# Kernel optimization log

Hardware: AMD Instinct MI355X
Metric: run time of the kernel (lower is better)

## Reference

```python
import math
import jax, jax.numpy as jnp
import numpy as np

B, QDIM, KDIM, EMBED, HEADS, H, W = 2, 192, 192, 256, 8, 48, 48


def setup_inputs() -> dict:
    key = jax.random.key(0)
    ks = jax.random.split(key, 8)
    s = 0.05
    return {
        "query": jax.random.normal(ks[0], (B, QDIM, H, W), dtype=jnp.float32),
        "key": jax.random.normal(ks[1], (B, KDIM, H, W), dtype=jnp.float32),
        "Wq": jax.random.normal(ks[2], (EMBED, QDIM), dtype=jnp.float32) * s,
        "bq": jax.random.normal(ks[3], (EMBED,), dtype=jnp.float32) * s,
        "Wk": jax.random.normal(ks[4], (EMBED, KDIM), dtype=jnp.float32) * s,
        "bk": jax.random.normal(ks[5], (EMBED,), dtype=jnp.float32) * s,
        "Wv": jax.random.normal(ks[6], (EMBED, KDIM), dtype=jnp.float32) * s,
        "bv": jax.random.normal(ks[7], (EMBED,), dtype=jnp.float32) * s,
        "num_heads": HEADS,
    }


def reference(query, key, Wq, bq, Wk, bk, Wv, bv, num_heads):
    b, qdim, h, w = query.shape
    L = h * w
    embed = Wq.shape[0]
    hd = embed // num_heads

    # (B, C, H, W) -> (B, L, C) raster order
    q = query.transpose(0, 2, 3, 1).reshape(b, L, qdim)
    k_in = key.transpose(0, 2, 3, 1).reshape(b, L, -1)

    q = q @ Wq.T + bq               # (B, L, E)
    v = k_in @ Wv.T + bv            # (B, L, E)
    k = k_in @ Wk.T + bk            # (B, L, E)

    q = q.reshape(b, L, num_heads, hd).transpose(0, 2, 1, 3)  # bhqd
    k = k.reshape(b, L, num_heads, hd).transpose(0, 2, 1, 3)  # bhkd
    v = v.reshape(b, L, num_heads, hd).transpose(0, 2, 1, 3)  # bhkd

    scores = jnp.einsum("bhqd,bhkd->bhqk", q, k) / math.sqrt(hd)
    # causal (square subsequent) mask: -inf strictly above diagonal
    idx = jnp.arange(L)
    neg = jnp.asarray(jnp.finfo(scores.dtype).min, scores.dtype)
    mask = jnp.where(idx[:, None] >= idx[None, :], jnp.zeros((), scores.dtype), neg)
    scores = scores + mask

    attn = jax.nn.softmax(scores, axis=-1)  # dropout p=0.0 (eval)
    x = jnp.einsum("bhqk,bhkd->bhqd", attn, v)  # (B, H, L, hd)

    # (B, H, L, hd) -> (B, H, hd, L) -> (B, E, h, w)
    out = x.transpose(0, 1, 3, 2).reshape(b, embed, h, w)
    return out
```

## Files before the change

### kernel.cpp

```cpp
#include <hip/hip_runtime.h>

#define LQ 2304
#define CIN 192
#define EMB 256
#define NH 8
#define HD 32

typedef __attribute__((ext_vector_type(8))) short short8;
typedef __attribute__((ext_vector_type(4))) short short4v;
typedef __attribute__((ext_vector_type(4))) float floatx4;
typedef __attribute__((ext_vector_type(16))) float f32x16;

__device__ __forceinline__ unsigned short f2bf(float f) {
  union { float f; unsigned u; } v; v.f = f;
  unsigned r = v.u + 0x7FFFu + ((v.u >> 16) & 1u);
  return (unsigned short)(r >> 16);
}
__device__ __forceinline__ unsigned cvtpk(float lo, float hi) {
  unsigned r;
  asm("v_cvt_pk_bf16_f32 %0, %1, %2" : "=v"(r) : "v"(lo), "v"(hi));
  return r;
}
__device__ __forceinline__ void plswap(unsigned& a, unsigned& b, int hi) {
#if __has_builtin(__builtin_amdgcn_permlane32_swap)
  auto r = __builtin_amdgcn_permlane32_swap((int)a, (int)b, false, false);
  a = (unsigned)r[0]; b = (unsigned)r[1];
#else
  unsigned pa = (unsigned)__shfl_xor((int)a, 32);
  unsigned pb = (unsigned)__shfl_xor((int)b, 32);
  unsigned na = hi ? pb : a;
  unsigned nb = hi ? b : pa;
  a = na; b = nb;
#endif
}
__device__ __forceinline__ float xmax(float x, int hi) {
  unsigned a = __float_as_uint(x), b = a;
  plswap(a, b, hi);
  return fmaxf(__uint_as_float(a), __uint_as_float(b));
}
__device__ __forceinline__ float xadd(float x, int hi) {
  unsigned a = __float_as_uint(x), b = a;
  plswap(a, b, hi);
  return __uint_as_float(a) + __uint_as_float(b);
}

__global__ void k_prep(const float* __restrict__ q, const float* __restrict__ k,
                       const float* __restrict__ Wq, const float* __restrict__ Wk,
                       const float* __restrict__ Wv,
                       unsigned short* Xtq, unsigned short* Xtk,
                       unsigned short* Wqb, unsigned short* Wkb, unsigned short* Wvb) {
  if (blockIdx.z == 2) {
    const int n = EMB * CIN;
    int i = (blockIdx.x + 108 * blockIdx.y) * 256 + threadIdx.x;
    if (i < n) { Wqb[i] = f2bf(Wq[i]); Wkb[i] = f2bf(Wk[i]); Wvb[i] = f2bf(Wv[i]); }
    return;
  }
  __shared__ float tile[64][65];
  const float* src = blockIdx.z ? k : q;
  unsigned short* dst = blockIdx.z ? Xtk : Xtq;
  int b = blockIdx.y;
  int lt = blockIdx.x % 36, ct = blockIdx.x / 36;
  int l0 = lt * 64, c0 = ct * 64;
  int j = threadIdx.x & 63, i0 = threadIdx.x >> 6;
  const float* s = src + (size_t)b * CIN * LQ;
  for (int i = i0; i < 64; i += 4)
    tile[i][j] = s[(size_t)(c0 + i) * LQ + l0 + j];
  __syncthreads();
  unsigned short* d = dst + (size_t)b * LQ * CIN;
  for (int li = i0; li < 64; li += 4)
    d[(size_t)(l0 + li) * CIN + c0 + j] = f2bf(tile[j][li]);
}

__global__ __launch_bounds__(256) void k_proj(
    const unsigned short* __restrict__ Xtq, const unsigned short* __restrict__ Xtk,
    const unsigned short* __restrict__ Wqb, const unsigned short* __restrict__ Wkb,
    const unsigned short* __restrict__ Wvb,
    const float* __restrict__ bq, const float* __restrict__ bk, const float* __restrict__ bv,
    unsigned short* Qb, unsigned short* Kb, unsigned short* Vt) {
  int proj = blockIdx.z;
  int b = blockIdx.y;
  int l0 = blockIdx.x * 16;
  const unsigned short* Xt = (proj == 0) ? Xtq : Xtk;
  const unsigned short* W  = (proj == 0) ? Wqb : (proj == 1 ? Wkb : Wvb);
  const float* bias        = (proj == 0) ? bq  : (proj == 1 ? bk  : bv);
  const float alpha = (proj == 0) ? 0.25505653582177047f : 1.0f;

  int lane = threadIdx.x & 63, w = threadIdx.x >> 6;
  int g = lane >> 4, r16 = lane & 15;
  int e0 = w * 64;
  int lg = l0 + r16;

  floatx4 acc[4];
  #pragma unroll
  for (int a = 0; a < 4; ++a) acc[a] = (floatx4){0.f, 0.f, 0.f, 0.f};

  const unsigned short* xrow = Xt + ((size_t)b * LQ + lg) * CIN + g * 8;
  #pragma unroll
  for (int ks = 0; ks < CIN; ks += 32) {
    short8 xf = *(const short8*)(xrow + ks);
    #pragma unroll
    for (int a = 0; a < 4; ++a) {
      short8 wf = *(const short8*)(W + (size_t)(e0 + a * 16 + r16) * CIN + ks + g * 8);
      acc[a] = __builtin_amdgcn_mfma_f32_16x16x32_bf16(wf, xf, acc[a], 0, 0, 0);
    }
  }

  #pragma unroll
  for (int a = 0; a < 4; ++a) {
    int ebase = e0 + a * 16 + g * 4;
    int h = ebase >> 5, d0 = ebase & 31;
    if (proj < 2) {
      unsigned short* outp = (proj == 0) ? Qb : Kb;
      short4v pk;
      #pragma unroll
      for (int r = 0; r < 4; ++r)
        pk[r] = (short)f2bf((acc[a][r] + bias[ebase + r]) * alpha);
      *(short4v*)(outp + ((size_t)(b * NH + h) * LQ + lg) * HD + d0) = pk;
    } else {
      #pragma unroll
      for (int r = 0; r < 4; ++r)
        Vt[((size_t)(b * NH + h) * HD + d0 + r) * LQ + lg] =
            f2bf(acc[a][r] + bias[ebase + r]);
    }
  }
}

__global__ __launch_bounds__(256, 3) void k_attn(const unsigned short* __restrict__ Qb,
                                                 const unsigned short* __restrict__ Kb,
                                                 const unsigned short* __restrict__ Vt,
                                                 float* __restrict__ out) {
  __shared__ float Osh[4][32][33];
  __shared__ float Msh[4][32];
  __shared__ float Ssh[4][32];

  int bid = blockIdx.x;
  int xcd = bid & 7;
  int idx = bid >> 3;
  int half = idx / 72;
  int j = 71 - (idx - half * 72);
  int bh = xcd + 8 * half;
  int q0b = j * 32;

  int w = threadIdx.x >> 6, lane = threadIdx.x & 63;
  int qcol = lane & 31, hi = lane >> 5;
  int qg = q0b + qcol;

  const unsigned short* Qrow = Qb + ((size_t)bh * LQ + qg) * HD + hi * 8;
  short8 qf0 = *(const short8*)(Qrow);
  short8 qf1 = *(const short8*)(Qrow + 16);

  const f32x16 Z16 = {0,0,0,0,0,0,0,0,0,0,0,0,0,0,0,0};
  f32x16 O = Z16;
  float m = -1e30f, sum = 0.f;

  const unsigned short* Kbase = Kb + (size_t)bh * LQ * HD;
  const unsigned short* Vbase = Vt + (size_t)bh * HD * LQ;
  int ntiles = (q0b + 95) >> 6;

  int t = w;
  short8 kf[4];
  if (t < ntiles) {
    const unsigned short* kr = Kbase + (size_t)(t * 64 + qcol) * HD + hi * 8;
    kf[0] = *(const short8*)(kr);
    kf[1] = *(const short8*)(kr + 16);
    kf[2] = *(const short8*)(kr + 32 * HD);
    kf[3] = *(const short8*)(kr + 32 * HD + 16);
  }

  while (t < ntiles) {
    int k0 = t * 64;
    int tn = t + 4;
    int kpre = ((tn < ntiles) ? tn : t) * 64;

    short8 kn[4];
    {
      const unsigned short* kr = Kbase + (size_t)(kpre + qcol) * HD + hi * 8;
      kn[0] = *(const short8*)(kr);
      kn[1] = *(const short8*)(kr + 16);
      kn[2] = *(const short8*)(kr + 32 * HD);
      kn[3] = *(const short8*)(kr + 32 * HD + 16);
    }
    short8 vf[4];
    {
      const unsigned short* vr = Vbase + (size_t)qcol * LQ + k0 + hi * 8;
      vf[0] = *(const short8*)(vr);
      vf[1] = *(const short8*)(vr + 16);
      vf[2] = *(const short8*)(vr + 32);
      vf[3] = *(const short8*)(vr + 48);
    }

    __builtin_amdgcn_s_setprio(1);
    f32x16 c0 = __builtin_amdgcn_mfma_f32_32x32x16_bf16(kf[0], qf0, Z16, 0, 0, 0);
    c0 = __builtin_amdgcn_mfma_f32_32x32x16_bf16(kf[1], qf1, c0, 0, 0, 0);
    f32x16 c1 = __builtin_amdgcn_mfma_f32_32x32x16_bf16(kf[2], qf0, Z16, 0, 0, 0);
    c1 = __builtin_amdgcn_mfma_f32_32x32x16_bf16(kf[3], qf1, c1, 0, 0, 0);
    __builtin_amdgcn_s_setprio(0);

    if (t == ntiles - 1) {
      #pragma unroll
      for (int i = 0; i < 16; ++i) {
        int kg = k0 + (i & 3) + 8 * (i >> 2) + 4 * hi;
        if (kg > qg)      c0[i] = -1e30f;
        if (kg + 32 > qg) c1[i] = -1e30f;
      }
    }

    float mx;
    {
      float a0 = fmaxf(fmaxf(c0[0], c0[8]),  fmaxf(c1[0], c1[8]));
      float a1 = fmaxf(fmaxf(c0[1], c0[9]),  fmaxf(c1[1], c1[9]));
      float a2 = fmaxf(fmaxf(c0[2], c0[10]), fmaxf(c1[2], c1[10]));
      float a3 = fmaxf(fmaxf(c0[3], c0[11]), fmaxf(c1[3], c1[11]));
      float a4 = fmaxf(fmaxf(c0[4], c0[12]), fmaxf(c1[4], c1[12]));
      float a5 = fmaxf(fmaxf(c0[5], c0[13]), fmaxf(c1[5], c1[13]));
      float a6 = fmaxf(fmaxf(c0[6], c0[14]), fmaxf(c1[6], c1[14]));
      float a7 = fmaxf(fmaxf(c0[7], c0[15]), fmaxf(c1[7], c1[15]));
      mx = fmaxf(fmaxf(fmaxf(a0, a1), fmaxf(a2, a3)),
                 fmaxf(fmaxf(a4, a5), fmaxf(a6, a7)));
    }
    mx = xmax(mx, hi);

    if (!__all(mx - m <= 8.0f)) {
      float mn = fmaxf(m, mx);
      float al = exp2f(m - mn);
      sum *= al;
      #pragma unroll
      for (int i = 0; i < 16; ++i) O[i] *= al;
      m = mn;
    }

    #pragma unroll
    for (int i = 0; i < 16; ++i) {
      c0[i] = exp2f(c0[i] - m);
      c1[i] = exp2f(c1[i] - m);
    }
    {
      float a0 = (c0[0] + c0[8])  + (c1[0] + c1[8]);
      float a1 = (c0[1] + c0[9])  + (c1[1] + c1[9]);
      float a2 = (c0[2] + c0[10]) + (c1[2] + c1[10]);
      float a3 = (c0[3] + c0[11]) + (c1[3] + c1[11]);
      float a4 = (c0[4] + c0[12]) + (c1[4] + c1[12]);
      float a5 = (c0[5] + c0[13]) + (c1[5] + c1[13]);
      float a6 = (c0[6] + c0[14]) + (c1[6] + c1[14]);
      float a7 = (c0[7] + c0[15]) + (c1[7] + c1[15]);
      float ts = ((a0 + a1) + (a2 + a3)) + ((a4 + a5) + (a6 + a7));
      sum += xadd(ts, hi);
    }

    union { unsigned u[4]; short8 s; } pA, pB, pC, pD;
    {
      unsigned a = cvtpk(c0[0], c0[1]), b = cvtpk(c0[2], c0[3]);
      unsigned c = cvtpk(c0[4], c0[5]), d = cvtpk(c0[6], c0[7]);
      plswap(a, c, hi); plswap(b, d, hi);
      pA.u[0] = a; pA.u[1] = b; pA.u[2] = c; pA.u[3] = d;
    }
    {
      unsigned a = cvtpk(c0[8], c0[9]),  b = cvtpk(c0[10], c0[11]);
      unsigned c = cvtpk(c0[12], c0[13]), d = cvtpk(c0[14], c0[15]);
      plswap(a, c, hi); plswap(b, d, hi);
      pB.u[0] = a; pB.u[1] = b; pB.u[2] = c; pB.u[3] = d;
    }
    {
      unsigned a = cvtpk(c1[0], c1[1]), b = cvtpk(c1[2], c1[3]);
      unsigned c = cvtpk(c1[4], c1[5]), d = cvtpk(c1[6], c1[7]);
      plswap(a, c, hi); plswap(b, d, hi);
      pC.u[0] = a; pC.u[1] = b; pC.u[2] = c; pC.u[3] = d;
    }
    {
      unsigned a = cvtpk(c1[8], c1[9]),  b = cvtpk(c1[10], c1[11]);
      unsigned c = cvtpk(c1[12], c1[13]), d = cvtpk(c1[14], c1[15]);
      plswap(a, c, hi); plswap(b, d, hi);
      pD.u[0] = a; pD.u[1] = b; pD.u[2] = c; pD.u[3] = d;
    }

    __builtin_amdgcn_s_setprio(1);
    O = __builtin_amdgcn_mfma_f32_32x32x16_bf16(vf[0], pA.s, O, 0, 0, 0);
    O = __builtin_amdgcn_mfma_f32_32x32x16_bf16(vf[1], pB.s, O, 0, 0, 0);
    O = __builtin_amdgcn_mfma_f32_32x32x16_bf16(vf[2], pC.s, O, 0, 0, 0);
    O = __builtin_amdgcn_mfma_f32_32x32x16_bf16(vf[3], pD.s, O, 0, 0, 0);
    __builtin_amdgcn_s_setprio(0);

    kf[0] = kn[0]; kf[1] = kn[1]; kf[2] = kn[2]; kf[3] = kn[3];
    t = tn;
  }

  #pragma unroll
  for (int i = 0; i < 16; ++i) {
    int d = (i & 3) + 8 * (i >> 2) + 4 * hi;
    Osh[w][d][qcol] = O[i];
  }
  if (hi == 0) { Msh[w][qcol] = m; Ssh[w][qcol] = sum; }
  __syncthreads();

  int tid = threadIdx.x;
  int q = tid & 31, dblk = tid >> 5;
  float m0 = Msh[0][q], m1 = Msh[1][q], m2 = Msh[2][q], m3 = Msh[3][q];
  float ms = fmaxf(fmaxf(m0, m1), fmaxf(m2, m3));
  float a0 = exp2f(m0 - ms), a1 = exp2f(m1 - ms);
  float a2 = exp2f(m2 - ms), a3 = exp2f(m3 - ms);
  float ss = a0 * Ssh[0][q] + a1 * Ssh[1][q] + a2 * Ssh[2][q] + a3 * Ssh[3][q];
  float inv = 1.0f / ss;
  #pragma unroll
  for (int r = 0; r < 4; ++r) {
    int d = dblk * 4 + r;
    float o = a0 * Osh[0][d][q] + a1 * Osh[1][d][q] +
              a2 * Osh[2][d][q] + a3 * Osh[3][d][q];
    out[((size_t)bh * HD + d) * LQ + q0b + q] = o * inv;
  }
}

extern "C" void kernel_launch(void* const* d_in, const int* in_sizes, int n_in,
                              void* d_out, int out_size, void* d_ws, size_t ws_size,
                              hipStream_t stream) {
  const float* query = (const float*)d_in[0];
  const float* key   = (const float*)d_in[1];
  const float* Wq    = (const float*)d_in[2];
  const float* bq    = (const float*)d_in[3];
  const float* Wk    = (const float*)d_in[4];
  const float* bk    = (const float*)d_in[5];
  const float* Wv    = (const float*)d_in[6];
  const float* bv    = (const float*)d_in[7];
  float* out = (float*)d_out;

  unsigned short* Wqb = (unsigned short*)d_ws;
  unsigned short* Wkb = Wqb + EMB * CIN;
  unsigned short* Wvb = Wkb + EMB * CIN;
  unsigned short* Xtq = Wvb + EMB * CIN;
  unsigned short* Xtk = Xtq + 2 * LQ * CIN;
  unsigned short* Qb  = Xtk + 2 * LQ * CIN;
  unsigned short* Kb  = Qb + 2 * NH * LQ * HD;
  unsigned short* Vt  = Kb + 2 * NH * LQ * HD;

  hipLaunchKernelGGL(k_prep, dim3(108, 2, 3), dim3(256), 0, stream,
                     query, key, Wq, Wk, Wv, Xtq, Xtk, Wqb, Wkb, Wvb);
  hipLaunchKernelGGL(k_proj, dim3(144, 2, 3), dim3(256), 0, stream,
                     Xtq, Xtk, Wqb, Wkb, Wvb, bq, bk, bv, Qb, Kb, Vt);
  hipLaunchKernelGGL(k_attn, dim3(1152), dim3(256), 0, stream,
                     Qb, Kb, Vt, out);
}
```

Baseline: 51.00 us.

## Process 64 queries per attention block to reuse K/V fragments across two query tiles

Each attention workgroup now handles two 32-row query sub-tiles (64 queries) instead of one. Every K and V fragment loaded from global memory feeds both sub-tiles, so K/V load traffic per query is halved, and the grid shrinks from 1152 to 576 blocks. The cost is twice the accumulator and softmax state per thread, which raises register pressure and may hurt occupancy. Fewer, larger blocks can also worsen load balance across CUs under the causal workload.

```diff
diff --git a/kernel.cpp b/kernel.cpp
--- a/kernel.cpp
+++ b/kernel.cpp
@@ -125,37 +125,121 @@
   }
 }
 
+__device__ __forceinline__ void softmax_pv(f32x16& c0, f32x16& c1, f32x16& O,
+                                           float& m, float& sum,
+                                           const short8* vf, int hi) {
+  const f32x16 Z16 = {0,0,0,0,0,0,0,0,0,0,0,0,0,0,0,0};
+  (void)Z16;
+  float mx;
+  {
+    float a0 = fmaxf(fmaxf(c0[0], c0[8]),  fmaxf(c1[0], c1[8]));
+    float a1 = fmaxf(fmaxf(c0[1], c0[9]),  fmaxf(c1[1], c1[9]));
+    float a2 = fmaxf(fmaxf(c0[2], c0[10]), fmaxf(c1[2], c1[10]));
+    float a3 = fmaxf(fmaxf(c0[3], c0[11]), fmaxf(c1[3], c1[11]));
+    float a4 = fmaxf(fmaxf(c0[4], c0[12]), fmaxf(c1[4], c1[12]));
+    float a5 = fmaxf(fmaxf(c0[5], c0[13]), fmaxf(c1[5], c1[13]));
+    float a6 = fmaxf(fmaxf(c0[6], c0[14]), fmaxf(c1[6], c1[14]));
+    float a7 = fmaxf(fmaxf(c0[7], c0[15]), fmaxf(c1[7], c1[15]));
+    mx = fmaxf(fmaxf(fmaxf(a0, a1), fmaxf(a2, a3)),
+               fmaxf(fmaxf(a4, a5), fmaxf(a6, a7)));
+  }
+  mx = xmax(mx, hi);
+
+  if (!__all(mx - m <= 8.0f)) {
+    float mn = fmaxf(m, mx);
+    float al = exp2f(m - mn);
+    sum *= al;
+    #pragma unroll
+    for (int i = 0; i < 16; ++i) O[i] *= al;
+    m = mn;
+  }
+
+  #pragma unroll
+  for (int i = 0; i < 16; ++i) {
+    c0[i] = exp2f(c0[i] - m);
+    c1[i] = exp2f(c1[i] - m);
+  }
+  {
+    float a0 = (c0[0] + c0[8])  + (c1[0] + c1[8]);
+    float a1 = (c0[1] + c0[9])  + (c1[1] + c1[9]);
+    float a2 = (c0[2] + c0[10]) + (c1[2] + c1[10]);
+    float a3 = (c0[3] + c0[11]) + (c1[3] + c1[11]);
+    float a4 = (c0[4] + c0[12]) + (c1[4] + c1[12]);
+    float a5 = (c0[5] + c0[13]) + (c1[5] + c1[13]);
+    float a6 = (c0[6] + c0[14]) + (c1[6] + c1[14]);
+    float a7 = (c0[7] + c0[15]) + (c1[7] + c1[15]);
+    float ts = ((a0 + a1) + (a2 + a3)) + ((a4 + a5) + (a6 + a7));
+    sum += xadd(ts, hi);
+  }
+
+  union { unsigned u[4]; short8 s; } pA, pB, pC, pD;
+  {
+    unsigned a = cvtpk(c0[0], c0[1]), b = cvtpk(c0[2], c0[3]);
+    unsigned c = cvtpk(c0[4], c0[5]), d = cvtpk(c0[6], c0[7]);
+    plswap(a, c, hi); plswap(b, d, hi);
+    pA.u[0] = a; pA.u[1] = b; pA.u[2] = c; pA.u[3] = d;
+  }
+  {
+    unsigned a = cvtpk(c0[8], c0[9]),  b = cvtpk(c0[10], c0[11]);
+    unsigned c = cvtpk(c0[12], c0[13]), d = cvtpk(c0[14], c0[15]);
+    plswap(a, c, hi); plswap(b, d, hi);
+    pB.u[0] = a; pB.u[1] = b; pB.u[2] = c; pB.u[3] = d;
+  }
+  {
+    unsigned a = cvtpk(c1[0], c1[1]), b = cvtpk(c1[2], c1[3]);
+    unsigned c = cvtpk(c1[4], c1[5]), d = cvtpk(c1[6], c1[7]);
+    plswap(a, c, hi); plswap(b, d, hi);
+    pC.u[0] = a; pC.u[1] = b; pC.u[2] = c; pC.u[3] = d;
+  }
+  {
+    unsigned a = cvtpk(c1[8], c1[9]),  b = cvtpk(c1[10], c1[11]);
+    unsigned c = cvtpk(c1[12], c1[13]), d = cvtpk(c1[14], c1[15]);
+    plswap(a, c, hi); plswap(b, d, hi);
+    pD.u[0] = a; pD.u[1] = b; pD.u[2] = c; pD.u[3] = d;
+  }
+
+  __builtin_amdgcn_s_setprio(1);
+  O = __builtin_amdgcn_mfma_f32_32x32x16_bf16(vf[0], pA.s, O, 0, 0, 0);
+  O = __builtin_amdgcn_mfma_f32_32x32x16_bf16(vf[1], pB.s, O, 0, 0, 0);
+  O = __builtin_amdgcn_mfma_f32_32x32x16_bf16(vf[2], pC.s, O, 0, 0, 0);
+  O = __builtin_amdgcn_mfma_f32_32x32x16_bf16(vf[3], pD.s, O, 0, 0, 0);
+  __builtin_amdgcn_s_setprio(0);
+}
+
 __global__ __launch_bounds__(256, 3) void k_attn(const unsigned short* __restrict__ Qb,
                                                  const unsigned short* __restrict__ Kb,
                                                  const unsigned short* __restrict__ Vt,
                                                  float* __restrict__ out) {
-  __shared__ float Osh[4][32][33];
-  __shared__ float Msh[4][32];
-  __shared__ float Ssh[4][32];
+  __shared__ float Osh[4][32][65];
+  __shared__ float Msh[4][64];
+  __shared__ float Ssh[4][64];
 
   int bid = blockIdx.x;
   int xcd = bid & 7;
   int idx = bid >> 3;
-  int half = idx / 72;
-  int j = 71 - (idx - half * 72);
+  int half = idx / 36;
+  int j = 35 - (idx - half * 36);
   int bh = xcd + 8 * half;
-  int q0b = j * 32;
+  int q0b = j * 64;
+  int ntiles = j + 1;
 
   int w = threadIdx.x >> 6, lane = threadIdx.x & 63;
   int qcol = lane & 31, hi = lane >> 5;
-  int qg = q0b + qcol;
-
-  const unsigned short* Qrow = Qb + ((size_t)bh * LQ + qg) * HD + hi * 8;
-  short8 qf0 = *(const short8*)(Qrow);
-  short8 qf1 = *(const short8*)(Qrow + 16);
+  int qgA = q0b + qcol, qgB = q0b + 32 + qcol;
+
+  const unsigned short* QrowA = Qb + ((size_t)bh * LQ + qgA) * HD + hi * 8;
+  const unsigned short* QrowB = Qb + ((size_t)bh * LQ + qgB) * HD + hi * 8;
+  short8 qfA0 = *(const short8*)(QrowA);
+  short8 qfA1 = *(const short8*)(QrowA + 16);
+  short8 qfB0 = *(const short8*)(QrowB);
+  short8 qfB1 = *(const short8*)(QrowB + 16);
 
   const f32x16 Z16 = {0,0,0,0,0,0,0,0,0,0,0,0,0,0,0,0};
-  f32x16 O = Z16;
-  float m = -1e30f, sum = 0.f;
+  f32x16 OA = Z16, OB = Z16;
+  float mA = -1e30f, sA = 0.f, mB = -1e30f, sB = 0.f;
 
   const unsigned short* Kbase = Kb + (size_t)bh * LQ * HD;
   const unsigned short* Vbase = Vt + (size_t)bh * HD * LQ;
-  int ntiles = (q0b + 95) >> 6;
 
   int t = w;
   short8 kf[4];
@@ -188,97 +272,42 @@
       vf[2] = *(const short8*)(vr + 32);
       vf[3] = *(const short8*)(vr + 48);
     }
-
-    __builtin_amdgcn_s_setprio(1);
-    f32x16 c0 = __builtin_amdgcn_mfma_f32_32x32x16_bf16(kf[0], qf0, Z16, 0, 0, 0);
-    c0 = __builtin_amdgcn_mfma_f32_32x32x16_bf16(kf[1], qf1, c0, 0, 0, 0);
-    f32x16 c1 = __builtin_amdgcn_mfma_f32_32x32x16_bf16(kf[2], qf0, Z16, 0, 0, 0);
-    c1 = __builtin_amdgcn_mfma_f32_32x32x16_bf16(kf[3], qf1, c1, 0, 0, 0);
-    __builtin_amdgcn_s_setprio(0);
-
-    if (t == ntiles - 1) {
-      #pragma unroll
-      for (int i = 0; i < 16; ++i) {
-        int kg = k0 + (i & 3) + 8 * (i >> 2) + 4 * hi;
-        if (kg > qg)      c0[i] = -1e30f;
-        if (kg + 32 > qg) c1[i] = -1e30f;
+    bool diag = (t == ntiles - 1);
+
+    {
+      __builtin_amdgcn_s_setprio(1);
+      f32x16 c0 = __builtin_amdgcn_mfma_f32_32x32x16_bf16(kf[0], qfA0, Z16, 0, 0, 0);
+      c0 = __builtin_amdgcn_mfma_f32_32x32x16_bf16(kf[1], qfA1, c0, 0, 0, 0);
+      f32x16 c1 = __builtin_amdgcn_mfma_f32_32x32x16_bf16(kf[2], qfA0, Z16, 0, 0, 0);
+      c1 = __builtin_amdgcn_mfma_f32_32x32x16_bf16(kf[3], qfA1, c1, 0, 0, 0);
+      __builtin_amdgcn_s_setprio(0);
+      if (diag) {
+        #pragma unroll
+        for (int i = 0; i < 16; ++i) {
+          int kg = k0 + (i & 3) + 8 * (i >> 2) + 4 * hi;
+          if (kg > qgA)      c0[i] = -1e30f;
+          if (kg + 32 > qgA) c1[i] = -1e30f;
+        }
       }
-    }
-
-    float mx;
+      softmax_pv(c0, c1, OA, mA, sA, vf, hi);
+    }
     {
-      float a0 = fmaxf(fmaxf(c0[0], c0[8]),  fmaxf(c1[0], c1[8]));
-      float a1 = fmaxf(fmaxf(c0[1], c0[9]),  fmaxf(c1[1], c1[9]));
-      float a2 = fmaxf(fmaxf(c0[2], c0[10]), fmaxf(c1[2], c1[10]));
-      float a3 = fmaxf(fmaxf(c0[3], c0[11]), fmaxf(c1[3], c1[11]));
-      float a4 = fmaxf(fmaxf(c0[4], c0[12]), fmaxf(c1[4], c1[12]));
-      float a5 = fmaxf(fmaxf(c0[5], c0[13]), fmaxf(c1[5], c1[13]));
-      float a6 = fmaxf(fmaxf(c0[6], c0[14]), fmaxf(c1[6], c1[14]));
-      float a7 = fmaxf(fmaxf(c0[7], c0[15]), fmaxf(c1[7], c1[15]));
-      mx = fmaxf(fmaxf(fmaxf(a0, a1), fmaxf(a2, a3)),
-                 fmaxf(fmaxf(a4, a5), fmaxf(a6, a7)));
-    }
-    mx = xmax(mx, hi);
-
-    if (!__all(mx - m <= 8.0f)) {
-      float mn = fmaxf(m, mx);
-      float al = exp2f(m - mn);
-      sum *= al;
-      #pragma unroll
-      for (int i = 0; i < 16; ++i) O[i] *= al;
-      m = mn;
-    }
-
-    #pragma unroll
-    for (int i = 0; i < 16; ++i) {
-      c0[i] = exp2f(c0[i] - m);
-      c1[i] = exp2f(c1[i] - m);
-    }
-    {
-      float a0 = (c0[0] + c0[8])  + (c1[0] + c1[8]);
-      float a1 = (c0[1] + c0[9])  + (c1[1] + c1[9]);
-      float a2 = (c0[2] + c0[10]) + (c1[2] + c1[10]);
-      float a3 = (c0[3] + c0[11]) + (c1[3] + c1[11]);
-      float a4 = (c0[4] + c0[12]) + (c1[4] + c1[12]);
-      float a5 = (c0[5] + c0[13]) + (c1[5] + c1[13]);
-      float a6 = (c0[6] + c0[14]) + (c1[6] + c1[14]);
-      float a7 = (c0[7] + c0[15]) + (c1[7] + c1[15]);
-      float ts = ((a0 + a1) + (a2 + a3)) + ((a4 + a5) + (a6 + a7));
-      sum += xadd(ts, hi);
-    }
-
-    union { unsigned u[4]; short8 s; } pA, pB, pC, pD;
-    {
-      unsigned a = cvtpk(c0[0], c0[1]), b = cvtpk(c0[2], c0[3]);
-      unsigned c = cvtpk(c0[4], c0[5]), d = cvtpk(c0[6], c0[7]);
-      plswap(a, c, hi); plswap(b, d, hi);
-      pA.u[0] = a; pA.u[1] = b; pA.u[2] = c; pA.u[3] = d;
-    }
-    {
-      unsigned a = cvtpk(c0[8], c0[9]),  b = cvtpk(c0[10], c0[11]);
-      unsigned c = cvtpk(c0[12], c0[13]), d = cvtpk(c0[14], c0[15]);
-      plswap(a, c, hi); plswap(b, d, hi);
-      pB.u[0] = a; pB.u[1] = b; pB.u[2] = c; pB.u[3] = d;
-    }
-    {
-      unsigned a = cvtpk(c1[0], c1[1]), b = cvtpk(c1[2], c1[3]);
-      unsigned c = cvtpk(c1[4], c1[5]), d = cvtpk(c1[6], c1[7]);
-      plswap(a, c, hi); plswap(b, d, hi);
-      pC.u[0] = a; pC.u[1] = b; pC.u[2] = c; pC.u[3] = d;
-    }
-    {
-      unsigned a = cvtpk(c1[8], c1[9]),  b = cvtpk(c1[10], c1[11]);
-      unsigned c = cvtpk(c1[12], c1[13]), d = cvtpk(c1[14], c1[15]);
-      plswap(a, c, hi); plswap(b, d, hi);
-      pD.u[0] = a; pD.u[1] = b; pD.u[2] = c; pD.u[3] = d;
-    }
-
-    __builtin_amdgcn_s_setprio(1);
-    O = __builtin_amdgcn_mfma_f32_32x32x16_bf16(vf[0], pA.s, O, 0, 0, 0);
-    O = __builtin_amdgcn_mfma_f32_32x32x16_bf16(vf[1], pB.s, O, 0, 0, 0);
-    O = __builtin_amdgcn_mfma_f32_32x32x16_bf16(vf[2], pC.s, O, 0, 0, 0);
-    O = __builtin_amdgcn_mfma_f32_32x32x16_bf16(vf[3], pD.s, O, 0, 0, 0);
-    __builtin_amdgcn_s_setprio(0);
+      __builtin_amdgcn_s_setprio(1);
+      f32x16 c0 = __builtin_amdgcn_mfma_f32_32x32x16_bf16(kf[0], qfB0, Z16, 0, 0, 0);
+      c0 = __builtin_amdgcn_mfma_f32_32x32x16_bf16(kf[1], qfB1, c0, 0, 0, 0);
+      f32x16 c1 = __builtin_amdgcn_mfma_f32_32x32x16_bf16(kf[2], qfB0, Z16, 0, 0, 0);
+      c1 = __builtin_amdgcn_mfma_f32_32x32x16_bf16(kf[3], qfB1, c1, 0, 0, 0);
+      __builtin_amdgcn_s_setprio(0);
+      if (diag) {
+        #pragma unroll
+        for (int i = 0; i < 16; ++i) {
+          int kg = k0 + (i & 3) + 8 * (i >> 2) + 4 * hi;
+          if (kg > qgB)      c0[i] = -1e30f;
+          if (kg + 32 > qgB) c1[i] = -1e30f;
+        }
+      }
+      softmax_pv(c0, c1, OB, mB, sB, vf, hi);
+    }
 
     kf[0] = kn[0]; kf[1] = kn[1]; kf[2] = kn[2]; kf[3] = kn[3];
     t = tn;
@@ -287,13 +316,16 @@
   #pragma unroll
   for (int i = 0; i < 16; ++i) {
     int d = (i & 3) + 8 * (i >> 2) + 4 * hi;
-    Osh[w][d][qcol] = O[i];
-  }
-  if (hi == 0) { Msh[w][qcol] = m; Ssh[w][qcol] = sum; }
+    Osh[w][d][qcol] = OA[i];
+    Osh[w][d][32 + qcol] = OB[i];
+  }
+  if (hi == 0) {
+    Msh[w][qcol] = mA; Ssh[w][qcol] = sA;
+    Msh[w][32 + qcol] = mB; Ssh[w][32 + qcol] = sB;
+  }
   __syncthreads();
 
-  int tid = threadIdx.x;
-  int q = tid & 31, dblk = tid >> 5;
+  int q = threadIdx.x & 63, dblk = threadIdx.x >> 6;
   float m0 = Msh[0][q], m1 = Msh[1][q], m2 = Msh[2][q], m3 = Msh[3][q];
   float ms = fmaxf(fmaxf(m0, m1), fmaxf(m2, m3));
   float a0 = exp2f(m0 - ms), a1 = exp2f(m1 - ms);
@@ -301,8 +333,8 @@
   float ss = a0 * Ssh[0][q] + a1 * Ssh[1][q] + a2 * Ssh[2][q] + a3 * Ssh[3][q];
   float inv = 1.0f / ss;
   #pragma unroll
-  for (int r = 0; r < 4; ++r) {
-    int d = dblk * 4 + r;
+  for (int r = 0; r < 8; ++r) {
+    int d = dblk * 8 + r;
     float o = a0 * Osh[0][d][q] + a1 * Osh[1][d][q] +
               a2 * Osh[2][d][q] + a3 * Osh[3][d][q];
     out[((size_t)bh * HD + d) * LQ + q0b + q] = o * inv;
@@ -335,6 +367,6 @@
                      query, key, Wq, Wk, Wv, Xtq, Xtk, Wqb, Wkb, Wvb);
   hipLaunchKernelGGL(k_proj, dim3(144, 2, 3), dim3(256), 0, stream,
                      Xtq, Xtk, Wqb, Wkb, Wvb, bq, bk, bv, Qb, Kb, Vt);
-  hipLaunchKernelGGL(k_attn, dim3(1152), dim3(256), 0, stream,
+  hipLaunchKernelGGL(k_attn, dim3(576), dim3(256), 0, stream,
                      Qb, Kb, Vt, out);
 }
```

Result: slower. 60.72 us (+19.1%).

## Fuse input transpose/bf16 conversion into QKV projection and drop K prefetch

Applied to the files above, without the earlier changes.

Merges the prep kernel (transpose and bf16 conversion of inputs and weights) into the projection kernel. Each block now transposes a 64-row input tile into LDS and converts fp32 weights to bf16 on the fly, removing one launch and the round trip of intermediate buffers through global memory. Each block also computes 64 rows instead of 16, so weights are reused across four row subtiles. In attention, the software prefetch of the next K tile is removed to cut register use, and launch bounds move to 4 blocks per CU. The trade-off is that each projection block converts weights redundantly and K loads are no longer hidden behind compute.

```diff
diff --git a/kernel.cpp b/kernel.cpp
--- a/kernel.cpp
+++ b/kernel.cpp
@@ -44,64 +44,67 @@
   return __uint_as_float(a) + __uint_as_float(b);
 }
 
-__global__ void k_prep(const float* __restrict__ q, const float* __restrict__ k,
-                       const float* __restrict__ Wq, const float* __restrict__ Wk,
-                       const float* __restrict__ Wv,
-                       unsigned short* Xtq, unsigned short* Xtk,
-                       unsigned short* Wqb, unsigned short* Wkb, unsigned short* Wvb) {
-  if (blockIdx.z == 2) {
-    const int n = EMB * CIN;
-    int i = (blockIdx.x + 108 * blockIdx.y) * 256 + threadIdx.x;
-    if (i < n) { Wqb[i] = f2bf(Wq[i]); Wkb[i] = f2bf(Wk[i]); Wvb[i] = f2bf(Wv[i]); }
-    return;
-  }
-  __shared__ float tile[64][65];
-  const float* src = blockIdx.z ? k : q;
-  unsigned short* dst = blockIdx.z ? Xtk : Xtq;
-  int b = blockIdx.y;
-  int lt = blockIdx.x % 36, ct = blockIdx.x / 36;
-  int l0 = lt * 64, c0 = ct * 64;
-  int j = threadIdx.x & 63, i0 = threadIdx.x >> 6;
-  const float* s = src + (size_t)b * CIN * LQ;
-  for (int i = i0; i < 64; i += 4)
-    tile[i][j] = s[(size_t)(c0 + i) * LQ + l0 + j];
-  __syncthreads();
-  unsigned short* d = dst + (size_t)b * LQ * CIN;
-  for (int li = i0; li < 64; li += 4)
-    d[(size_t)(l0 + li) * CIN + c0 + j] = f2bf(tile[j][li]);
-}
-
-__global__ __launch_bounds__(256) void k_proj(
-    const unsigned short* __restrict__ Xtq, const unsigned short* __restrict__ Xtk,
-    const unsigned short* __restrict__ Wqb, const unsigned short* __restrict__ Wkb,
-    const unsigned short* __restrict__ Wvb,
+__global__ __launch_bounds__(256) void k_qkv(
+    const float* __restrict__ query, const float* __restrict__ key,
+    const float* __restrict__ Wq, const float* __restrict__ Wk, const float* __restrict__ Wv,
     const float* __restrict__ bq, const float* __restrict__ bk, const float* __restrict__ bv,
     unsigned short* Qb, unsigned short* Kb, unsigned short* Vt) {
+  __shared__ float tile[64][65];
+  __shared__ unsigned short Xs[64][200];
+
   int proj = blockIdx.z;
   int b = blockIdx.y;
-  int l0 = blockIdx.x * 16;
-  const unsigned short* Xt = (proj == 0) ? Xtq : Xtk;
-  const unsigned short* W  = (proj == 0) ? Wqb : (proj == 1 ? Wkb : Wvb);
-  const float* bias        = (proj == 0) ? bq  : (proj == 1 ? bk  : bv);
+  int l0 = blockIdx.x * 64;
+  const float* src  = (proj == 0) ? query : key;
+  const float* Wf   = (proj == 0) ? Wq : (proj == 1 ? Wk : Wv);
+  const float* bias = (proj == 0) ? bq : (proj == 1 ? bk : bv);
   const float alpha = (proj == 0) ? 0.25505653582177047f : 1.0f;
 
-  int lane = threadIdx.x & 63, w = threadIdx.x >> 6;
+  int tid = threadIdx.x;
+  int j = tid & 63, i0 = tid >> 6;
+  const float* sp = src + (size_t)b * CIN * LQ;
+
+  for (int ch = 0; ch < 3; ++ch) {
+    int c0 = ch * 64;
+    #pragma unroll
+    for (int i = i0; i < 64; i += 4)
+      tile[i][j] = sp[(size_t)(c0 + i) * LQ + l0 + j];
+    __syncthreads();
+    #pragma unroll
+    for (int li = i0; li < 64; li += 4)
+      Xs[li][c0 + j] = f2bf(tile[j][li]);
+    __syncthreads();
+  }
+
+  int lane = tid & 63, w = tid >> 6;
   int g = lane >> 4, r16 = lane & 15;
   int e0 = w * 64;
-  int lg = l0 + r16;
-
-  floatx4 acc[4];
-  #pragma unroll
-  for (int a = 0; a < 4; ++a) acc[a] = (floatx4){0.f, 0.f, 0.f, 0.f};
-
-  const unsigned short* xrow = Xt + ((size_t)b * LQ + lg) * CIN + g * 8;
+
+  floatx4 acc[4][4];
+  #pragma unroll
+  for (int a = 0; a < 4; ++a)
+    #pragma unroll
+    for (int ls = 0; ls < 4; ++ls) acc[a][ls] = (floatx4){0.f, 0.f, 0.f, 0.f};
+
   #pragma unroll
   for (int ks = 0; ks < CIN; ks += 32) {
-    short8 xf = *(const short8*)(xrow + ks);
+    short8 wf[4];
     #pragma unroll
     for (int a = 0; a < 4; ++a) {
-      short8 wf = *(const short8*)(W + (size_t)(e0 + a * 16 + r16) * CIN + ks + g * 8);
-      acc[a] = __builtin_amdgcn_mfma_f32_16x16x32_bf16(wf, xf, acc[a], 0, 0, 0);
+      const float* wp = Wf + (size_t)(e0 + a * 16 + r16) * CIN + ks + g * 8;
+      union { unsigned u[4]; short8 s; } pk;
+      pk.u[0] = cvtpk(wp[0], wp[1]);
+      pk.u[1] = cvtpk(wp[2], wp[3]);
+      pk.u[2] = cvtpk(wp[4], wp[5]);
+      pk.u[3] = cvtpk(wp[6], wp[7]);
+      wf[a] = pk.s;
+    }
+    #pragma unroll
+    for (int ls = 0; ls < 4; ++ls) {
+      short8 xf = *(const short8*)&Xs[ls * 16 + r16][ks + g * 8];
+      #pragma unroll
+      for (int a = 0; a < 4; ++a)
+        acc[a][ls] = __builtin_amdgcn_mfma_f32_16x16x32_bf16(wf[a], xf, acc[a][ls], 0, 0, 0);
     }
   }
 
@@ -109,23 +112,106 @@
   for (int a = 0; a < 4; ++a) {
     int ebase = e0 + a * 16 + g * 4;
     int h = ebase >> 5, d0 = ebase & 31;
-    if (proj < 2) {
-      unsigned short* outp = (proj == 0) ? Qb : Kb;
-      short4v pk;
-      #pragma unroll
-      for (int r = 0; r < 4; ++r)
-        pk[r] = (short)f2bf((acc[a][r] + bias[ebase + r]) * alpha);
-      *(short4v*)(outp + ((size_t)(b * NH + h) * LQ + lg) * HD + d0) = pk;
-    } else {
-      #pragma unroll
-      for (int r = 0; r < 4; ++r)
-        Vt[((size_t)(b * NH + h) * HD + d0 + r) * LQ + lg] =
-            f2bf(acc[a][r] + bias[ebase + r]);
-    }
-  }
-}
-
-__global__ __launch_bounds__(256, 3) void k_attn(const unsigned short* __restrict__ Qb,
+    #pragma unroll
+    for (int ls = 0; ls < 4; ++ls) {
+      int lg = l0 + ls * 16 + r16;
+      if (proj < 2) {
+        unsigned short* outp = (proj == 0) ? Qb : Kb;
+        short4v pk;
+        #pragma unroll
+        for (int r = 0; r < 4; ++r)
+          pk[r] = (short)f2bf((acc[a][ls][r] + bias[ebase + r]) * alpha);
+        *(short4v*)(outp + ((size_t)(b * NH + h) * LQ + lg) * HD + d0) = pk;
+      } else {
+        #pragma unroll
+        for (int r = 0; r < 4; ++r)
+          Vt[((size_t)(b * NH + h) * HD + d0 + r) * LQ + lg] =
+              f2bf(acc[a][ls][r] + bias[ebase + r]);
+      }
+    }
+  }
+}
+
+__device__ __forceinline__ void softmax_pv(f32x16& c0, f32x16& c1, f32x16& O,
+                                           float& m, float& sum,
+                                           const short8* vf, int hi) {
+  float mx;
+  {
+    float a0 = fmaxf(fmaxf(c0[0], c0[8]),  fmaxf(c1[0], c1[8]));
+    float a1 = fmaxf(fmaxf(c0[1], c0[9]),  fmaxf(c1[1], c1[9]));
+    float a2 = fmaxf(fmaxf(c0[2], c0[10]), fmaxf(c1[2], c1[10]));
+    float a3 = fmaxf(fmaxf(c0[3], c0[11]), fmaxf(c1[3], c1[11]));
+    float a4 = fmaxf(fmaxf(c0[4], c0[12]), fmaxf(c1[4], c1[12]));
+    float a5 = fmaxf(fmaxf(c0[5], c0[13]), fmaxf(c1[5], c1[13]));
+    float a6 = fmaxf(fmaxf(c0[6], c0[14]), fmaxf(c1[6], c1[14]));
+    float a7 = fmaxf(fmaxf(c0[7], c0[15]), fmaxf(c1[7], c1[15]));
+    mx = fmaxf(fmaxf(fmaxf(a0, a1), fmaxf(a2, a3)),
+               fmaxf(fmaxf(a4, a5), fmaxf(a6, a7)));
+  }
+  mx = xmax(mx, hi);
+
+  if (!__all(mx - m <= 8.0f)) {
+    float mn = fmaxf(m, mx);
+    float al = exp2f(m - mn);
+    sum *= al;
+    #pragma unroll
+    for (int i = 0; i < 16; ++i) O[i] *= al;
+    m = mn;
+  }
+
+  #pragma unroll
+  for (int i = 0; i < 16; ++i) {
+    c0[i] = exp2f(c0[i] - m);
+    c1[i] = exp2f(c1[i] - m);
+  }
+  {
+    float a0 = (c0[0] + c0[8])  + (c1[0] + c1[8]);
+    float a1 = (c0[1] + c0[9])  + (c1[1] + c1[9]);
+    float a2 = (c0[2] + c0[10]) + (c1[2] + c1[10]);
+    float a3 = (c0[3] + c0[11]) + (c1[3] + c1[11]);
+    float a4 = (c0[4] + c0[12]) + (c1[4] + c1[12]);
+    float a5 = (c0[5] + c0[13]) + (c1[5] + c1[13]);
+    float a6 = (c0[6] + c0[14]) + (c1[6] + c1[14]);
+    float a7 = (c0[7] + c0[15]) + (c1[7] + c1[15]);
+    float ts = ((a0 + a1) + (a2 + a3)) + ((a4 + a5) + (a6 + a7));
+    sum += xadd(ts, hi);
+  }
+
+  union { unsigned u[4]; short8 s; } pA, pB, pC, pD;
+  {
+    unsigned a = cvtpk(c0[0], c0[1]), b = cvtpk(c0[2], c0[3]);
+    unsigned c = cvtpk(c0[4], c0[5]), d = cvtpk(c0[6], c0[7]);
+    plswap(a, c, hi); plswap(b, d, hi);
+    pA.u[0] = a; pA.u[1] = b; pA.u[2] = c; pA.u[3] = d;
+  }
+  {
+    unsigned a = cvtpk(c0[8], c0[9]),  b = cvtpk(c0[10], c0[11]);
+    unsigned c = cvtpk(c0[12], c0[13]), d = cvtpk(c0[14], c0[15]);
+    plswap(a, c, hi); plswap(b, d, hi);
+    pB.u[0] = a; pB.u[1] = b; pB.u[2] = c; pB.u[3] = d;
+  }
+  {
+    unsigned a = cvtpk(c1[0], c1[1]), b = cvtpk(c1[2], c1[3]);
+    unsigned c = cvtpk(c1[4], c1[5]), d = cvtpk(c1[6], c1[7]);
+    plswap(a, c, hi); plswap(b, d, hi);
+    pC.u[0] = a; pC.u[1] = b; pC.u[2] = c; pC.u[3] = d;
+  }
+  {
+    unsigned a = cvtpk(c1[8], c1[9]),  b = cvtpk(c1[10], c1[11]);
+    unsigned c = cvtpk(c1[12], c1[13]), d = cvtpk(c1[14], c1[15]);
+    plswap(a, c, hi); plswap(b, d, hi);
+    pD.u[0] = a; pD.u[1] = b; pD.u[2] = c; pD.u[3] = d;
+  }
+
+  __builtin_amdgcn_s_setprio(1);
+  O = __builtin_amdgcn_mfma_f32_32x32x16_bf16(vf[0], pA.s, O, 0, 0, 0);
+  O = __builtin_amdgcn_mfma_f32_32x32x16_bf16(vf[1], pB.s, O, 0, 0, 0);
+  O = __builtin_amdgcn_mfma_f32_32x32x16_bf16(vf[2], pC.s, O, 0, 0, 0);
+  O = __builtin_amdgcn_mfma_f32_32x32x16_bf16(vf[3], pD.s, O, 0, 0, 0);
+  __builtin_amdgcn_s_setprio(0);
+}
+
+__global__ __launch_bounds__(256, 4) void k_attn(const unsigned short* __restrict__ Qb,
                                                  const unsigned short* __restrict__ Kb,
                                                  const unsigned short* __restrict__ Vt,
                                                  float* __restrict__ out) {
@@ -157,31 +243,16 @@
   const unsigned short* Vbase = Vt + (size_t)bh * HD * LQ;
   int ntiles = (q0b + 95) >> 6;
 
-  int t = w;
-  short8 kf[4];
-  if (t < ntiles) {
-    const unsigned short* kr = Kbase + (size_t)(t * 64 + qcol) * HD + hi * 8;
-    kf[0] = *(const short8*)(kr);
-    kf[1] = *(const short8*)(kr + 16);
-    kf[2] = *(const short8*)(kr + 32 * HD);
-    kf[3] = *(const short8*)(kr + 32 * HD + 16);
-  }
-
-  while (t < ntiles) {
+  for (int t = w; t < ntiles; t += 4) {
     int k0 = t * 64;
-    int tn = t + 4;
-    int kpre = ((tn < ntiles) ? tn : t) * 64;
-
-    short8 kn[4];
+
+    short8 kf[4], vf[4];
     {
-      const unsigned short* kr = Kbase + (size_t)(kpre + qcol) * HD + hi * 8;
-      kn[0] = *(const short8*)(kr);
-      kn[1] = *(const short8*)(kr + 16);
-      kn[2] = *(const short8*)(kr + 32 * HD);
-      kn[3] = *(const short8*)(kr + 32 * HD + 16);
-    }
-    short8 vf[4];
-    {
+      const unsigned short* kr = Kbase + (size_t)(k0 + qcol) * HD + hi * 8;
+      kf[0] = *(const short8*)(kr);
+      kf[1] = *(const short8*)(kr + 16);
+      kf[2] = *(const short8*)(kr + 32 * HD);
+      kf[3] = *(const short8*)(kr + 32 * HD + 16);
       const unsigned short* vr = Vbase + (size_t)qcol * LQ + k0 + hi * 8;
       vf[0] = *(const short8*)(vr);
       vf[1] = *(const short8*)(vr + 16);
@@ -205,83 +276,7 @@
       }
     }
 
-    float mx;
-    {
-      float a0 = fmaxf(fmaxf(c0[0], c0[8]),  fmaxf(c1[0], c1[8]));
-      float a1 = fmaxf(fmaxf(c0[1], c0[9]),  fmaxf(c1[1], c1[9]));
-      float a2 = fmaxf(fmaxf(c0[2], c0[10]), fmaxf(c1[2], c1[10]));
-      float a3 = fmaxf(fmaxf(c0[3], c0[11]), fmaxf(c1[3], c1[11]));
-      float a4 = fmaxf(fmaxf(c0[4], c0[12]), fmaxf(c1[4], c1[12]));
-      float a5 = fmaxf(fmaxf(c0[5], c0[13]), fmaxf(c1[5], c1[13]));
-      float a6 = fmaxf(fmaxf(c0[6], c0[14]), fmaxf(c1[6], c1[14]));
-      float a7 = fmaxf(fmaxf(c0[7], c0[15]), fmaxf(c1[7], c1[15]));
-      mx = fmaxf(fmaxf(fmaxf(a0, a1), fmaxf(a2, a3)),
-                 fmaxf(fmaxf(a4, a5), fmaxf(a6, a7)));
-    }
-    mx = xmax(mx, hi);
-
-    if (!__all(mx - m <= 8.0f)) {
-      float mn = fmaxf(m, mx);
-      float al = exp2f(m - mn);
-      sum *= al;
-      #pragma unroll
-      for (int i = 0; i < 16; ++i) O[i] *= al;
-      m = mn;
-    }
-
-    #pragma unroll
-    for (int i = 0; i < 16; ++i) {
-      c0[i] = exp2f(c0[i] - m);
-      c1[i] = exp2f(c1[i] - m);
-    }
-    {
-      float a0 = (c0[0] + c0[8])  + (c1[0] + c1[8]);
-      float a1 = (c0[1] + c0[9])  + (c1[1] + c1[9]);
-      float a2 = (c0[2] + c0[10]) + (c1[2] + c1[10]);
-      float a3 = (c0[3] + c0[11]) + (c1[3] + c1[11]);
-      float a4 = (c0[4] + c0[12]) + (c1[4] + c1[12]);
-      float a5 = (c0[5] + c0[13]) + (c1[5] + c1[13]);
-      float a6 = (c0[6] + c0[14]) + (c1[6] + c1[14]);
-      float a7 = (c0[7] + c0[15]) + (c1[7] + c1[15]);
-      float ts = ((a0 + a1) + (a2 + a3)) + ((a4 + a5) + (a6 + a7));
-      sum += xadd(ts, hi);
-    }
-
-    union { unsigned u[4]; short8 s; } pA, pB, pC, pD;
-    {
-      unsigned a = cvtpk(c0[0], c0[1]), b = cvtpk(c0[2], c0[3]);
-      unsigned c = cvtpk(c0[4], c0[5]), d = cvtpk(c0[6], c0[7]);
-      plswap(a, c, hi); plswap(b, d, hi);
-      pA.u[0] = a; pA.u[1] = b; pA.u[2] = c; pA.u[3] = d;
-    }
-    {
-      unsigned a = cvtpk(c0[8], c0[9]),  b = cvtpk(c0[10], c0[11]);
-      unsigned c = cvtpk(c0[12], c0[13]), d = cvtpk(c0[14], c0[15]);
-      plswap(a, c, hi); plswap(b, d, hi);
-      pB.u[0] = a; pB.u[1] = b; pB.u[2] = c; pB.u[3] = d;
-    }
-    {
-      unsigned a = cvtpk(c1[0], c1[1]), b = cvtpk(c1[2], c1[3]);
-      unsigned c = cvtpk(c1[4], c1[5]), d = cvtpk(c1[6], c1[7]);
-      plswap(a, c, hi); plswap(b, d, hi);
-      pC.u[0] = a; pC.u[1] = b; pC.u[2] = c; pC.u[3] = d;
-    }
-    {
-      unsigned a = cvtpk(c1[8], c1[9]),  b = cvtpk(c1[10], c1[11]);
-      unsigned c = cvtpk(c1[12], c1[13]), d = cvtpk(c1[14], c1[15]);
-      plswap(a, c, hi); plswap(b, d, hi);
-      pD.u[0] = a; pD.u[1] = b; pD.u[2] = c; pD.u[3] = d;
-    }
-
-    __builtin_amdgcn_s_setprio(1);
-    O = __builtin_amdgcn_mfma_f32_32x32x16_bf16(vf[0], pA.s, O, 0, 0, 0);
-    O = __builtin_amdgcn_mfma_f32_32x32x16_bf16(vf[1], pB.s, O, 0, 0, 0);
-    O = __builtin_amdgcn_mfma_f32_32x32x16_bf16(vf[2], pC.s, O, 0, 0, 0);
-    O = __builtin_amdgcn_mfma_f32_32x32x16_bf16(vf[3], pD.s, O, 0, 0, 0);
-    __builtin_amdgcn_s_setprio(0);
-
-    kf[0] = kn[0]; kf[1] = kn[1]; kf[2] = kn[2]; kf[3] = kn[3];
-    t = tn;
+    softmax_pv(c0, c1, O, m, sum, vf, hi);
   }
 
   #pragma unroll
@@ -322,19 +317,12 @@
   const float* bv    = (const float*)d_in[7];
   float* out = (float*)d_out;
 
-  unsigned short* Wqb = (unsigned short*)d_ws;
-  unsigned short* Wkb = Wqb + EMB * CIN;
-  unsigned short* Wvb = Wkb + EMB * CIN;
-  unsigned short* Xtq = Wvb + EMB * CIN;
-  unsigned short* Xtk = Xtq + 2 * LQ * CIN;
-  unsigned short* Qb  = Xtk + 2 * LQ * CIN;
-  unsigned short* Kb  = Qb + 2 * NH * LQ * HD;
-  unsigned short* Vt  = Kb + 2 * NH * LQ * HD;
-
-  hipLaunchKernelGGL(k_prep, dim3(108, 2, 3), dim3(256), 0, stream,
-                     query, key, Wq, Wk, Wv, Xtq, Xtk, Wqb, Wkb, Wvb);
-  hipLaunchKernelGGL(k_proj, dim3(144, 2, 3), dim3(256), 0, stream,
-                     Xtq, Xtk, Wqb, Wkb, Wvb, bq, bk, bv, Qb, Kb, Vt);
+  unsigned short* Qb = (unsigned short*)d_ws;
+  unsigned short* Kb = Qb + 2 * NH * LQ * HD;
+  unsigned short* Vt = Kb + 2 * NH * LQ * HD;
+
+  hipLaunchKernelGGL(k_qkv, dim3(36, 2, 3), dim3(256), 0, stream,
+                     query, key, Wq, Wk, Wv, bq, bk, bv, Qb, Kb, Vt);
   hipLaunchKernelGGL(k_attn, dim3(1152), dim3(256), 0, stream,
                      Qb, Kb, Vt, out);
 }
```

Result: faster. 46.04 us (-9.7%).
